# Optimization experiments

Measured on AMD Instinct MI355X. Metric: run time of the kernel, lower is better.

## Reference

```python
import jax, jax.numpy as jnp
import numpy as np


def setup_inputs() -> dict:
    key = jax.random.key(0)
    ks = jax.random.split(key, 5)
    B, T, S, D = 4, 32, 320, 768
    return {
        "x": jax.random.normal(ks[0], (B, T, S, D), dtype=jnp.float32),
        "qkv_w": jax.random.normal(ks[1], (D, 3 * D), dtype=jnp.float32) * 0.02,
        "qkv_b": jax.random.normal(ks[2], (3 * D,), dtype=jnp.float32) * 0.02,
        "out_w": jax.random.normal(ks[3], (D, D), dtype=jnp.float32) * 0.02,
        "out_b": jax.random.normal(ks[4], (D,), dtype=jnp.float32) * 0.02,
        "n_latents": 64,
        "n_heads": 12,
    }


def reference(x, qkv_w, qkv_b, out_w, out_b, n_latents, n_heads):
    B, T, S, D = x.shape
    H = n_heads
    hd = D // H
    scale = 1.0 / jnp.sqrt(jnp.asarray(hd, dtype=x.dtype))

    # qkv projection: [B,T,S,3D]
    qkv = jnp.einsum('btsd,de->btse', x, qkv_w) + qkv_b
    q, k, v = jnp.split(qkv, 3, axis=-1)
    # [B,T,S,H,hd]
    q = q.reshape(B, T, S, H, hd)
    k = k.reshape(B, T, S, H, hd)
    v = v.reshape(B, T, S, H, hd)

    # block-sparse mask: latent queries (rows < n_latents) cannot attend to
    # patch keys (cols >= n_latents); everything else allowed
    rows = jnp.arange(S) < n_latents          # latent query rows
    cols = jnp.arange(S) >= n_latents         # patch key cols
    allow = ~(rows[:, None] & cols[None, :])  # [S,S] bool

    # attention scores [B,T,H,Sq,Sk]
    scores = jnp.einsum('btqhd,btkhd->bthqk', q, k) * scale
    scores = jnp.where(allow, scores, -jnp.inf)
    attn = jax.nn.softmax(scores, axis=-1)

    y = jnp.einsum('bthqk,btkhd->btqhd', attn, v).reshape(B, T, S, D)
    return jnp.einsum('btsd,de->btse', y, out_w) + out_b
```

## Files before the change

kernel.cpp:

```cpp
#include <hip/hip_runtime.h>

typedef __attribute__((ext_vector_type(8))) short bf16x8;
typedef __attribute__((ext_vector_type(4))) float f32x4;
typedef __attribute__((ext_vector_type(16))) float f32x16;
typedef __attribute__((address_space(1))) void gvoid_t;
typedef __attribute__((address_space(3))) void lvoid_t;

#define DEVI __device__ __forceinline__
#define SB __builtin_amdgcn_sched_barrier(0)

DEVI unsigned short f2bf(float f) {
    unsigned int u = __builtin_bit_cast(unsigned int, f);
    u += 0x7fffu + ((u >> 16) & 1u);
    return (unsigned short)(u >> 16);
}

DEVI unsigned cvt_pk_bf16(float a, float b) {
    unsigned r;
    asm("v_cvt_pk_bf16_f32 %0, %1, %2" : "=v"(r) : "v"(a), "v"(b));
    return r;
}

DEVI f32x4 mfma16(bf16x8 a, bf16x8 b, f32x4 c) {
    return __builtin_amdgcn_mfma_f32_16x16x32_bf16(a, b, c, 0, 0, 0);
}

__global__ void k_convert(const float* __restrict__ in, unsigned short* __restrict__ out, int n8) {
    int i = blockIdx.x * 256 + threadIdx.x;
    if (i >= n8) return;
    const float4* p = (const float4*)in + (size_t)i * 2;
    float4 a = p[0], b = p[1];
    uint4 o;
    o.x = f2bf(a.x) | ((unsigned)f2bf(a.y) << 16);
    o.y = f2bf(a.z) | ((unsigned)f2bf(a.w) << 16);
    o.z = f2bf(b.x) | ((unsigned)f2bf(b.y) << 16);
    o.w = f2bf(b.z) | ((unsigned)f2bf(b.w) << 16);
    *((uint4*)out + i) = o;
}

__global__ void k_transpose(const float* __restrict__ w, unsigned short* __restrict__ wt, int K, int N) {
    __shared__ float tile[32][33];
    int n0 = blockIdx.x * 32, k0 = blockIdx.y * 32;
    int tx = threadIdx.x, ty = threadIdx.y;
#pragma unroll
    for (int r = 0; r < 32; r += 8)
        tile[ty + r][tx] = w[(size_t)(k0 + ty + r) * N + n0 + tx];
    __syncthreads();
#pragma unroll
    for (int r = 0; r < 32; r += 8)
        wt[(size_t)(n0 + ty + r) * K + k0 + tx] = f2bf(tile[tx][ty + r]);
}

__global__ __launch_bounds__(256) void k_kpack(const unsigned short* __restrict__ qkv,
                                               unsigned short* __restrict__ kp) {
    int bht = blockIdx.x;
    int t = bht % 10, bh = bht / 10;
    int h = bh % 12, bt = bh / 12;
    int c = threadIdx.x >> 6, l = threadIdx.x & 63;
    const unsigned short* src = qkv + (size_t)(bt * 320 + t * 32 + (l & 31)) * 2304
                                + 768 + h * 64 + c * 16 + (l >> 5) * 8;
    uint4 v = *(const uint4*)src;
    *(uint4*)(kp + ((size_t)bht * 4 + c) * 512 + l * 8) = v;
}

template <bool OUT_BF16>
__global__ __launch_bounds__(512, 2) void k_gemm256(const unsigned short* __restrict__ A,
                                                    const unsigned short* __restrict__ Bt,
                                                    const float* __restrict__ bias,
                                                    void* __restrict__ out,
                                                    int M, int N, int K) {
    __shared__ unsigned short smem[65536];

    const int tid = threadIdx.x;
    const int nwg = gridDim.x, bid = blockIdx.x;
    const int q8 = nwg >> 3, r8 = nwg & 7;
    const int xcd = bid & 7, lid = bid >> 3;
    const int swz = ((xcd < r8) ? xcd * (q8 + 1) : r8 * (q8 + 1) + (xcd - r8) * q8) + lid;
    const int ntn = N >> 8;
    const int bm = swz / ntn, bn = swz % ntn;

    const int lane = tid & 63, wid = tid >> 6;
    const int wr = wid >> 2, wc = wid & 3;
    const int lr = lane & 15, lg = lane >> 4;
    const int cswz = (lr & 7) << 3;
    const int col0 = (lg * 8) ^ cswz;

    const int NT = K >> 6;

    const int srowl = tid >> 3;
    const int scole = ((tid & 7) ^ (srowl & 7)) << 3;
    const unsigned short* aSrc = A  + (size_t)(bm * 256 + srowl) * K + scole;
    const unsigned short* bSrc = Bt + (size_t)(bn * 256 + srowl) * K + scole;

#define STG(matOff, srcBase, qq, koff, bufw)                                              \
    __builtin_amdgcn_global_load_lds((gvoid_t*)((srcBase) + (size_t)(qq) * 64 * K + (koff)), \
        (lvoid_t*)(smem + (matOff) + (bufw) * 16384 + (qq) * 4096 + tid * 8), 16, 0, 0)
#define LDA(mf, base, rowoff, kk) \
    *(const bf16x8*)((base) + ((rowoff) + (mf) * 16 + lr) * 64 + (col0 ^ ((kk) * 32)))

    f32x4 acc[8][4];
#pragma unroll
    for (int i = 0; i < 8; ++i)
#pragma unroll
        for (int j = 0; j < 4; ++j) acc[i][j] = (f32x4){0.f, 0.f, 0.f, 0.f};

    {
        const int k1 = (NT > 1) ? 64 : 0;
        STG(0, aSrc, 0, 0, 0); STG(0, aSrc, 1, 0, 0); STG(0, aSrc, 2, 0, 0); STG(0, aSrc, 3, 0, 0);
        STG(32768, bSrc, 0, 0, 0); STG(32768, bSrc, 1, 0, 0); STG(32768, bSrc, 2, 0, 0); STG(32768, bSrc, 3, 0, 0);
        STG(0, aSrc, 0, k1, 1); STG(0, aSrc, 2, k1, 1);
        asm volatile("s_waitcnt vmcnt(2)" ::: "memory");
        __builtin_amdgcn_s_barrier();
    }

#pragma unroll 1
    for (int t = 0; t < NT; ++t) {
        const int bufR = t & 1, bufW = bufR ^ 1;
        const int ko1 = (t + 1 < NT) ? (t + 1) * 64 : 0;
        const int ko2 = (t + 2 < NT) ? (t + 2) * 64 : 0;
        const unsigned short* abuf = smem + bufR * 16384;
        const unsigned short* bbuf = smem + 32768 + bufR * 16384;
        bf16x8 afv[4][2], b01[2][2], b23[2][2];

#pragma unroll
        for (int j = 0; j < 2; ++j)
#pragma unroll
            for (int kk = 0; kk < 2; ++kk)
                b01[j][kk] = LDA(j, bbuf, wc * 64, kk);
#pragma unroll
        for (int mf = 0; mf < 2; ++mf)
#pragma unroll
            for (int kk = 0; kk < 2; ++kk)
                afv[mf][kk] = LDA(mf, abuf, wr * 128, kk);
        SB;
#pragma unroll
        for (int mf = 2; mf < 4; ++mf)
#pragma unroll
            for (int kk = 0; kk < 2; ++kk)
                afv[mf][kk] = LDA(mf, abuf, wr * 128, kk);
        SB;
        STG(32768, bSrc, 0, ko1, bufW); STG(32768, bSrc, 1, ko1, bufW);
        STG(32768, bSrc, 2, ko1, bufW); STG(32768, bSrc, 3, ko1, bufW);
        STG(0, aSrc, 1, ko1, bufW); STG(0, aSrc, 3, ko1, bufW);
        asm volatile("s_waitcnt lgkmcnt(4)" ::: "memory"); SB;
        __builtin_amdgcn_s_setprio(1);
#pragma unroll
        for (int mf = 0; mf < 2; ++mf)
#pragma unroll
            for (int j = 0; j < 2; ++j)
#pragma unroll
                for (int kk = 0; kk < 2; ++kk)
                    acc[mf][j] = mfma16(afv[mf][kk], b01[j][kk], acc[mf][j]);
        __builtin_amdgcn_s_setprio(0);
        asm volatile("s_waitcnt lgkmcnt(0)" ::: "memory"); SB;
        __builtin_amdgcn_s_setprio(1);
#pragma unroll
        for (int mf = 2; mf < 4; ++mf)
#pragma unroll
            for (int j = 0; j < 2; ++j)
#pragma unroll
                for (int kk = 0; kk < 2; ++kk)
                    acc[mf][j] = mfma16(afv[mf][kk], b01[j][kk], acc[mf][j]);
        __builtin_amdgcn_s_setprio(0);

#pragma unroll
        for (int kk = 0; kk < 2; ++kk)
            b23[0][kk] = LDA(2, bbuf, wc * 64, kk);
        SB;
#pragma unroll
        for (int kk = 0; kk < 2; ++kk)
            b23[1][kk] = LDA(3, bbuf, wc * 64, kk);
        SB;
        asm volatile("s_waitcnt lgkmcnt(2)" ::: "memory"); SB;
        __builtin_amdgcn_s_setprio(1);
#pragma unroll
        for (int mf = 0; mf < 4; ++mf)
#pragma unroll
            for (int kk = 0; kk < 2; ++kk)
                acc[mf][2] = mfma16(afv[mf][kk], b23[0][kk], acc[mf][2]);
        __builtin_amdgcn_s_setprio(0);
        asm volatile("s_waitcnt lgkmcnt(0)" ::: "memory"); SB;
        __builtin_amdgcn_s_setprio(1);
#pragma unroll
        for (int mf = 0; mf < 4; ++mf)
#pragma unroll
            for (int kk = 0; kk < 2; ++kk)
                acc[mf][3] = mfma16(afv[mf][kk], b23[1][kk], acc[mf][3]);
        __builtin_amdgcn_s_setprio(0);

#pragma unroll
        for (int mf = 0; mf < 2; ++mf)
#pragma unroll
            for (int kk = 0; kk < 2; ++kk)
                afv[mf][kk] = LDA(mf, abuf, wr * 128 + 64, kk);
        SB;
#pragma unroll
        for (int mf = 2; mf < 4; ++mf)
#pragma unroll
            for (int kk = 0; kk < 2; ++kk)
                afv[mf][kk] = LDA(mf, abuf, wr * 128 + 64, kk);
        SB;
        asm volatile("s_waitcnt lgkmcnt(4)" ::: "memory"); SB;
        __builtin_amdgcn_s_setprio(1);
#pragma unroll
        for (int mf = 0; mf < 2; ++mf)
#pragma unroll
            for (int j = 0; j < 2; ++j)
#pragma unroll
                for (int kk = 0; kk < 2; ++kk)
                    acc[4 + mf][2 + j] = mfma16(afv[mf][kk], b23[j][kk], acc[4 + mf][2 + j]);
        __builtin_amdgcn_s_setprio(0);
        asm volatile("s_waitcnt lgkmcnt(0)" ::: "memory"); SB;
        __builtin_amdgcn_s_setprio(1);
#pragma unroll
        for (int mf = 2; mf < 4; ++mf)
#pragma unroll
            for (int j = 0; j < 2; ++j)
#pragma unroll
                for (int kk = 0; kk < 2; ++kk)
                    acc[4 + mf][2 + j] = mfma16(afv[mf][kk], b23[j][kk], acc[4 + mf][2 + j]);
        __builtin_amdgcn_s_setprio(0);

        __builtin_amdgcn_s_setprio(1);
#pragma unroll
        for (int mf = 0; mf < 4; ++mf)
#pragma unroll
            for (int j = 0; j < 2; ++j)
#pragma unroll
                for (int kk = 0; kk < 2; ++kk)
                    acc[4 + mf][j] = mfma16(afv[mf][kk], b01[j][kk], acc[4 + mf][j]);
        __builtin_amdgcn_s_setprio(0);
        asm volatile("s_waitcnt vmcnt(0)" ::: "memory");
        __builtin_amdgcn_s_barrier();
        STG(0, aSrc, 0, ko2, bufR); STG(0, aSrc, 2, ko2, bufR);
    }
#undef STG
#undef LDA

    asm volatile("s_waitcnt vmcnt(0)" ::: "memory");
    __syncthreads();
    float bv[4];
#pragma unroll
    for (int nf = 0; nf < 4; ++nf)
        bv[nf] = bias[bn * 256 + wc * 64 + nf * 16 + lr];

    if (OUT_BF16) {
        unsigned short* ebuf = smem + wid * 8192;
#pragma unroll
        for (int h = 0; h < 2; ++h) {
#pragma unroll
            for (int mf4 = 0; mf4 < 4; ++mf4) {
                int mf = h * 4 + mf4;
#pragma unroll
                for (int nf = 0; nf < 4; ++nf)
#pragma unroll
                    for (int i = 0; i < 4; ++i)
                        ebuf[(mf4 * 16 + lg * 4 + i) * 72 + nf * 16 + lr] = f2bf(acc[mf][nf][i] + bv[nf]);
            }
            asm volatile("s_waitcnt lgkmcnt(0)" ::: "memory"); SB;
#pragma unroll
            for (int ps = 0; ps < 8; ++ps) {
                int rl = ps * 8 + (lane >> 3), ck = lane & 7;
                uint4 vv = *(const uint4*)&ebuf[rl * 72 + ck * 8];
                int grow = bm * 256 + wr * 128 + h * 64 + rl;
                int gcol = bn * 256 + wc * 64 + ck * 8;
                *(uint4*)&((unsigned short*)out)[(size_t)grow * N + gcol] = vv;
            }
            asm volatile("s_waitcnt lgkmcnt(0)" ::: "memory"); SB;
        }
    } else {
        float* ebuf = (float*)smem + wid * 4096;
#pragma unroll
        for (int qq = 0; qq < 4; ++qq) {
#pragma unroll
            for (int m2 = 0; m2 < 2; ++m2) {
                int mf = qq * 2 + m2;
#pragma unroll
                for (int nf = 0; nf < 4; ++nf)
#pragma unroll
                    for (int i = 0; i < 4; ++i)
                        ebuf[(m2 * 16 + lg * 4 + i) * 68 + nf * 16 + lr] = acc[mf][nf][i] + bv[nf];
            }
            asm volatile("s_waitcnt lgkmcnt(0)" ::: "memory"); SB;
#pragma unroll
            for (int ps = 0; ps < 8; ++ps) {
                int rl = ps * 4 + (lane >> 4), ck = lane & 15;
                uint4 vv = *(const uint4*)&ebuf[rl * 68 + ck * 4];
                int grow = bm * 256 + wr * 128 + qq * 32 + rl;
                int gcol = bn * 256 + wc * 64 + ck * 4;
                *(uint4*)&((float*)out)[(size_t)grow * N + gcol] = vv;
            }
            asm volatile("s_waitcnt lgkmcnt(0)" ::: "memory"); SB;
        }
    }
}

__global__ __launch_bounds__(640, 5) void k_attn6(const unsigned short* __restrict__ qkv,
                                                  const unsigned short* __restrict__ kp,
                                                  unsigned short* __restrict__ y) {
    int bt = blockIdx.x / 12, h = blockIdx.x % 12;
    const unsigned short* Qg = qkv + (size_t)bt * 320 * 2304 + h * 64;
    const unsigned short* Vg = Qg + 1536;
    const unsigned short* Kpb = kp + (size_t)blockIdx.x * 20480;

    __shared__ unsigned short Vt[10 * 64 * 40];

    int tid = threadIdx.x, w = tid >> 6, l = tid & 63;
    int q = l & 31, hh = l >> 5;
    int q0 = w * 32;
    int ntile = (w < 2) ? 2 : 10;

#pragma unroll
    for (int it = 0; it < 2; ++it) {
        int blk = tid + it * 640;
        int tt = blk >> 7, rr = blk & 127;
        int k0 = (rr & 7) * 4;
        int d0 = (rr >> 3) * 4;
        const unsigned short* src = Vg + (size_t)(tt * 32 + k0) * 2304 + d0;
        union { uint2 u; unsigned short s[4]; } r0, r1, r2, r3;
        r0.u = *(const uint2*)(src);
        r1.u = *(const uint2*)(src + 2304);
        r2.u = *(const uint2*)(src + 4608);
        r3.u = *(const uint2*)(src + 6912);
#pragma unroll
        for (int dd = 0; dd < 4; ++dd) {
            int d = d0 + dd;
            int sw = ((d >> 3) & 3) << 3;
            uint2 o;
            o.x = (unsigned)r0.s[dd] | ((unsigned)r1.s[dd] << 16);
            o.y = (unsigned)r2.s[dd] | ((unsigned)r3.s[dd] << 16);
            *(uint2*)&Vt[(size_t)(tt * 64 + d) * 40 + (k0 ^ sw)] = o;
        }
    }

    bf16x8 qf[4];
#pragma unroll
    for (int c = 0; c < 4; ++c)
        qf[c] = *(const bf16x8*)(Qg + (size_t)(q0 + q) * 2304 + c * 16 + hh * 8);

    f32x16 o0 = (f32x16)0.f, o1 = (f32x16)0.f;
    float m = -3e38f, lsum = 0.f;
    const float SC = 0.125f * 1.44269504089f;

    __syncthreads();

    for (int t = 0; t < ntile; ++t) {
        bf16x8 kf[4];
#pragma unroll
        for (int c = 0; c < 4; ++c)
            kf[c] = *(const bf16x8*)(Kpb + t * 2048 + c * 512 + l * 8);

        f32x16 sacc = (f32x16)0.f;
#pragma unroll
        for (int c = 0; c < 4; ++c)
            sacc = __builtin_amdgcn_mfma_f32_32x32x16_bf16(kf[c], qf[c], sacc, 0, 0, 0);

        float p[16];
#pragma unroll
        for (int r = 0; r < 16; ++r) p[r] = sacc[r] * SC;
        float tm = fmaxf(
            fmaxf(fmaxf(fmaxf(p[0], p[1]), fmaxf(p[2], p[3])),
                  fmaxf(fmaxf(p[4], p[5]), fmaxf(p[6], p[7]))),
            fmaxf(fmaxf(fmaxf(p[8], p[9]), fmaxf(p[10], p[11])),
                  fmaxf(fmaxf(p[12], p[13]), fmaxf(p[14], p[15]))));
        tm = fmaxf(tm, __shfl_xor(tm, 32));
        if (!__all(tm <= m + 8.f)) {
            float mn = fmaxf(m, tm);
            float al = __builtin_amdgcn_exp2f(m - mn);
            lsum *= al;
#pragma unroll
            for (int r = 0; r < 16; ++r) { o0[r] *= al; o1[r] *= al; }
            m = mn;
        }
#pragma unroll
        for (int r = 0; r < 16; ++r) p[r] = __builtin_amdgcn_exp2f(p[r] - m);
        float rs =
            ((p[0] + p[1]) + (p[2] + p[3])) + ((p[4] + p[5]) + (p[6] + p[7])) +
            (((p[8] + p[9]) + (p[10] + p[11])) + ((p[12] + p[13]) + (p[14] + p[15])));
        lsum += rs;

        unsigned a0 = cvt_pk_bf16(p[0], p[1]);
        unsigned a1 = cvt_pk_bf16(p[2], p[3]);
        unsigned b0 = cvt_pk_bf16(p[4], p[5]);
        unsigned b1 = cvt_pk_bf16(p[6], p[7]);
        asm("v_permlane32_swap_b32 %0, %1" : "+v"(a0), "+v"(b0));
        asm("v_permlane32_swap_b32 %0, %1" : "+v"(a1), "+v"(b1));
        unsigned c0 = cvt_pk_bf16(p[8], p[9]);
        unsigned c1 = cvt_pk_bf16(p[10], p[11]);
        unsigned d0 = cvt_pk_bf16(p[12], p[13]);
        unsigned d1 = cvt_pk_bf16(p[14], p[15]);
        asm("v_permlane32_swap_b32 %0, %1" : "+v"(c0), "+v"(d0));
        asm("v_permlane32_swap_b32 %0, %1" : "+v"(c1), "+v"(d1));
        union { unsigned u[4]; bf16x8 v; } pf0, pf1;
        pf0.u[0] = a0; pf0.u[1] = a1; pf0.u[2] = b0; pf0.u[3] = b1;
        pf1.u[0] = c0; pf1.u[1] = c1; pf1.u[2] = d0; pf1.u[3] = d1;

        const unsigned short* vt = Vt + t * 2560;
        {
            int d = q;
            int sw = (d >> 3) & 3;
            bf16x8 va0 = *(const bf16x8*)&vt[d * 40 + ((0 + hh) ^ sw) * 8];
            bf16x8 va1 = *(const bf16x8*)&vt[d * 40 + ((2 + hh) ^ sw) * 8];
            o0 = __builtin_amdgcn_mfma_f32_32x32x16_bf16(va0, pf0.v, o0, 0, 0, 0);
            o0 = __builtin_amdgcn_mfma_f32_32x32x16_bf16(va1, pf1.v, o0, 0, 0, 0);
        }
        {
            int d = 32 + q;
            int sw = (d >> 3) & 3;
            bf16x8 va0 = *(const bf16x8*)&vt[d * 40 + ((0 + hh) ^ sw) * 8];
            bf16x8 va1 = *(const bf16x8*)&vt[d * 40 + ((2 + hh) ^ sw) * 8];
            o1 = __builtin_amdgcn_mfma_f32_32x32x16_bf16(va0, pf0.v, o1, 0, 0, 0);
            o1 = __builtin_amdgcn_mfma_f32_32x32x16_bf16(va1, pf1.v, o1, 0, 0, 0);
        }
    }

    lsum += __shfl_xor(lsum, 32);
    float inv = 1.f / lsum;
    unsigned short* yp = y + (size_t)(bt * 320 + q0 + q) * 768 + h * 64;
#pragma unroll
    for (int r = 0; r < 16; r += 2) {
        int dr = (r & 3) + 8 * (r >> 2) + 4 * hh;
        *(unsigned*)(yp + dr) =
            (unsigned)f2bf(o0[r] * inv) | ((unsigned)f2bf(o0[r + 1] * inv) << 16);
        *(unsigned*)(yp + 32 + dr) =
            (unsigned)f2bf(o1[r] * inv) | ((unsigned)f2bf(o1[r + 1] * inv) << 16);
    }
}

extern "C" void kernel_launch(void* const* d_in, const int* in_sizes, int n_in,
                              void* d_out, int out_size, void* d_ws, size_t ws_size,
                              hipStream_t stream) {
    const float* x     = (const float*)d_in[0];
    const float* qkv_w = (const float*)d_in[1];
    const float* qkv_b = (const float*)d_in[2];
    const float* out_w = (const float*)d_in[3];
    const float* out_b = (const float*)d_in[4];

    const int M = 40960;
    unsigned short* xb  = (unsigned short*)d_ws;
    unsigned short* w1t = xb + (size_t)M * 768;
    unsigned short* w2t = w1t + (size_t)2304 * 768;
    unsigned short* qkv = w2t + (size_t)768 * 768;
    unsigned short* yb  = qkv + (size_t)M * 2304;
    unsigned short* kp  = xb;

    k_convert<<<(M * 768 / 8 + 255) / 256, 256, 0, stream>>>(x, xb, M * 768 / 8);
    k_transpose<<<dim3(2304 / 32, 768 / 32), dim3(32, 8), 0, stream>>>(qkv_w, w1t, 768, 2304);
    k_transpose<<<dim3(768 / 32, 768 / 32), dim3(32, 8), 0, stream>>>(out_w, w2t, 768, 768);

    k_gemm256<true><<<(M / 256) * (2304 / 256), 512, 0, stream>>>(xb, w1t, qkv_b, (void*)qkv, M, 2304, 768);
    k_kpack<<<1536 * 10, 256, 0, stream>>>(qkv, kp);
    k_attn6<<<128 * 12, 640, 0, stream>>>(qkv, kp, yb);
    k_gemm256<false><<<(M / 256) * (768 / 256), 512, 0, stream>>>(yb, w2t, out_b, d_out, M, 768, 768);
}
```

Before: 384.0 us.

## Restructure GEMM main loop with B-fragment prefetch and drop K-pack kernel

The GEMM inner loop is reorganised into a two-tile unrolled lambda. It loads all A-low fragments up front and prefetches the next tile's B0 fragments from the other LDS buffer after the barrier, so LDS reads overlap with MFMA work. Separately, the k_kpack launch is removed and the attention kernel reads K directly from the strided qkv buffer. This saves one kernel launch and a full pass over K, at the cost of less coalesced K loads inside attention. The unroll-by-two assumes NT is even (768/64=12), and holding more fragments live raises register pressure.

```diff
diff --git a/kernel.cpp b/kernel.cpp
--- a/kernel.cpp
+++ b/kernel.cpp
@@ -51,18 +51,6 @@
         wt[(size_t)(n0 + ty + r) * K + k0 + tx] = f2bf(tile[tx][ty + r]);
 }
 
-__global__ __launch_bounds__(256) void k_kpack(const unsigned short* __restrict__ qkv,
-                                               unsigned short* __restrict__ kp) {
-    int bht = blockIdx.x;
-    int t = bht % 10, bh = bht / 10;
-    int h = bh % 12, bt = bh / 12;
-    int c = threadIdx.x >> 6, l = threadIdx.x & 63;
-    const unsigned short* src = qkv + (size_t)(bt * 320 + t * 32 + (l & 31)) * 2304
-                                + 768 + h * 64 + c * 16 + (l >> 5) * 8;
-    uint4 v = *(const uint4*)src;
-    *(uint4*)(kp + ((size_t)bht * 4 + c) * 512 + l * 8) = v;
-}
-
 template <bool OUT_BF16>
 __global__ __launch_bounds__(512, 2) void k_gemm256(const unsigned short* __restrict__ A,
                                                     const unsigned short* __restrict__ Bt,
@@ -104,6 +92,8 @@
 #pragma unroll
         for (int j = 0; j < 4; ++j) acc[i][j] = (f32x4){0.f, 0.f, 0.f, 0.f};
 
+    bf16x8 b0A[2][2], b0B[2][2];
+
     {
         const int k1 = (NT > 1) ? 64 : 0;
         STG(0, aSrc, 0, 0, 0); STG(0, aSrc, 1, 0, 0); STG(0, aSrc, 2, 0, 0); STG(0, aSrc, 3, 0, 0);
@@ -111,33 +101,32 @@
         STG(0, aSrc, 0, k1, 1); STG(0, aSrc, 2, k1, 1);
         asm volatile("s_waitcnt vmcnt(2)" ::: "memory");
         __builtin_amdgcn_s_barrier();
-    }
-
-#pragma unroll 1
-    for (int t = 0; t < NT; ++t) {
+#pragma unroll
+        for (int j = 0; j < 2; ++j)
+#pragma unroll
+            for (int kk = 0; kk < 2; ++kk)
+                b0A[j][kk] = LDA(j, smem + 32768, wc * 64, kk);
+    }
+
+    auto TILE = [&](int t, bf16x8 (&b0c)[2][2], bf16x8 (&b0n)[2][2]) {
         const int bufR = t & 1, bufW = bufR ^ 1;
         const int ko1 = (t + 1 < NT) ? (t + 1) * 64 : 0;
         const int ko2 = (t + 2 < NT) ? (t + 2) * 64 : 0;
         const unsigned short* abuf = smem + bufR * 16384;
         const unsigned short* bbuf = smem + 32768 + bufR * 16384;
-        bf16x8 afv[4][2], b01[2][2], b23[2][2];
-
+        const unsigned short* bbufN = smem + 32768 + bufW * 16384;
+        bf16x8 a_lo[4][2], a_hi[4][2], b1[2][2];
+
+#pragma unroll
+        for (int mf = 0; mf < 4; ++mf)
+#pragma unroll
+            for (int kk = 0; kk < 2; ++kk)
+                a_lo[mf][kk] = LDA(mf, abuf, wr * 128, kk);
 #pragma unroll
         for (int j = 0; j < 2; ++j)
 #pragma unroll
             for (int kk = 0; kk < 2; ++kk)
-                b01[j][kk] = LDA(j, bbuf, wc * 64, kk);
-#pragma unroll
-        for (int mf = 0; mf < 2; ++mf)
-#pragma unroll
-            for (int kk = 0; kk < 2; ++kk)
-                afv[mf][kk] = LDA(mf, abuf, wr * 128, kk);
-        SB;
-#pragma unroll
-        for (int mf = 2; mf < 4; ++mf)
-#pragma unroll
-            for (int kk = 0; kk < 2; ++kk)
-                afv[mf][kk] = LDA(mf, abuf, wr * 128, kk);
+                b1[j][kk] = LDA(2 + j, bbuf, wc * 64, kk);
         SB;
         STG(32768, bSrc, 0, ko1, bufW); STG(32768, bSrc, 1, ko1, bufW);
         STG(32768, bSrc, 2, ko1, bufW); STG(32768, bSrc, 3, ko1, bufW);
@@ -145,99 +134,71 @@
         asm volatile("s_waitcnt lgkmcnt(4)" ::: "memory"); SB;
         __builtin_amdgcn_s_setprio(1);
 #pragma unroll
-        for (int mf = 0; mf < 2; ++mf)
+        for (int mf = 0; mf < 4; ++mf)
 #pragma unroll
             for (int j = 0; j < 2; ++j)
 #pragma unroll
                 for (int kk = 0; kk < 2; ++kk)
-                    acc[mf][j] = mfma16(afv[mf][kk], b01[j][kk], acc[mf][j]);
+                    acc[mf][j] = mfma16(a_lo[mf][kk], b0c[j][kk], acc[mf][j]);
         __builtin_amdgcn_s_setprio(0);
         asm volatile("s_waitcnt lgkmcnt(0)" ::: "memory"); SB;
+
+#pragma unroll
+        for (int mf = 0; mf < 4; ++mf)
+#pragma unroll
+            for (int kk = 0; kk < 2; ++kk)
+                a_hi[mf][kk] = LDA(mf, abuf, wr * 128 + 64, kk);
+        SB;
         __builtin_amdgcn_s_setprio(1);
 #pragma unroll
-        for (int mf = 2; mf < 4; ++mf)
+        for (int mf = 0; mf < 4; ++mf)
 #pragma unroll
             for (int j = 0; j < 2; ++j)
 #pragma unroll
                 for (int kk = 0; kk < 2; ++kk)
-                    acc[mf][j] = mfma16(afv[mf][kk], b01[j][kk], acc[mf][j]);
-        __builtin_amdgcn_s_setprio(0);
-
-#pragma unroll
-        for (int kk = 0; kk < 2; ++kk)
-            b23[0][kk] = LDA(2, bbuf, wc * 64, kk);
-        SB;
-#pragma unroll
-        for (int kk = 0; kk < 2; ++kk)
-            b23[1][kk] = LDA(3, bbuf, wc * 64, kk);
-        SB;
-        asm volatile("s_waitcnt lgkmcnt(2)" ::: "memory"); SB;
-        __builtin_amdgcn_s_setprio(1);
-#pragma unroll
-        for (int mf = 0; mf < 4; ++mf)
-#pragma unroll
-            for (int kk = 0; kk < 2; ++kk)
-                acc[mf][2] = mfma16(afv[mf][kk], b23[0][kk], acc[mf][2]);
+                    acc[mf][2 + j] = mfma16(a_lo[mf][kk], b1[j][kk], acc[mf][2 + j]);
         __builtin_amdgcn_s_setprio(0);
         asm volatile("s_waitcnt lgkmcnt(0)" ::: "memory"); SB;
+
         __builtin_amdgcn_s_setprio(1);
 #pragma unroll
         for (int mf = 0; mf < 4; ++mf)
 #pragma unroll
-            for (int kk = 0; kk < 2; ++kk)
-                acc[mf][3] = mfma16(afv[mf][kk], b23[1][kk], acc[mf][3]);
-        __builtin_amdgcn_s_setprio(0);
-
-#pragma unroll
-        for (int mf = 0; mf < 2; ++mf)
-#pragma unroll
-            for (int kk = 0; kk < 2; ++kk)
-                afv[mf][kk] = LDA(mf, abuf, wr * 128 + 64, kk);
-        SB;
-#pragma unroll
-        for (int mf = 2; mf < 4; ++mf)
-#pragma unroll
-            for (int kk = 0; kk < 2; ++kk)
-                afv[mf][kk] = LDA(mf, abuf, wr * 128 + 64, kk);
-        SB;
-        asm volatile("s_waitcnt lgkmcnt(4)" ::: "memory"); SB;
-        __builtin_amdgcn_s_setprio(1);
-#pragma unroll
-        for (int mf = 0; mf < 2; ++mf)
-#pragma unroll
             for (int j = 0; j < 2; ++j)
 #pragma unroll
                 for (int kk = 0; kk < 2; ++kk)
-                    acc[4 + mf][2 + j] = mfma16(afv[mf][kk], b23[j][kk], acc[4 + mf][2 + j]);
-        __builtin_amdgcn_s_setprio(0);
-        asm volatile("s_waitcnt lgkmcnt(0)" ::: "memory"); SB;
-        __builtin_amdgcn_s_setprio(1);
-#pragma unroll
-        for (int mf = 2; mf < 4; ++mf)
-#pragma unroll
-            for (int j = 0; j < 2; ++j)
-#pragma unroll
-                for (int kk = 0; kk < 2; ++kk)
-                    acc[4 + mf][2 + j] = mfma16(afv[mf][kk], b23[j][kk], acc[4 + mf][2 + j]);
-        __builtin_amdgcn_s_setprio(0);
-
-        __builtin_amdgcn_s_setprio(1);
-#pragma unroll
-        for (int mf = 0; mf < 4; ++mf)
-#pragma unroll
-            for (int j = 0; j < 2; ++j)
-#pragma unroll
-                for (int kk = 0; kk < 2; ++kk)
-                    acc[4 + mf][j] = mfma16(afv[mf][kk], b01[j][kk], acc[4 + mf][j]);
+                    acc[4 + mf][2 + j] = mfma16(a_hi[mf][kk], b1[j][kk], acc[4 + mf][2 + j]);
         __builtin_amdgcn_s_setprio(0);
         asm volatile("s_waitcnt vmcnt(0)" ::: "memory");
         __builtin_amdgcn_s_barrier();
+
+#pragma unroll
+        for (int j = 0; j < 2; ++j)
+#pragma unroll
+            for (int kk = 0; kk < 2; ++kk)
+                b0n[j][kk] = LDA(j, bbufN, wc * 64, kk);
+        SB;
         STG(0, aSrc, 0, ko2, bufR); STG(0, aSrc, 2, ko2, bufR);
+        __builtin_amdgcn_s_setprio(1);
+#pragma unroll
+        for (int mf = 0; mf < 4; ++mf)
+#pragma unroll
+            for (int j = 0; j < 2; ++j)
+#pragma unroll
+                for (int kk = 0; kk < 2; ++kk)
+                    acc[4 + mf][j] = mfma16(a_hi[mf][kk], b0c[j][kk], acc[4 + mf][j]);
+        __builtin_amdgcn_s_setprio(0);
+    };
+
+#pragma unroll 1
+    for (int t = 0; t < NT; t += 2) {
+        TILE(t, b0A, b0B);
+        TILE(t + 1, b0B, b0A);
     }
 #undef STG
 #undef LDA
 
-    asm volatile("s_waitcnt vmcnt(0)" ::: "memory");
+    asm volatile("s_waitcnt vmcnt(0) lgkmcnt(0)" ::: "memory");
     __syncthreads();
     float bv[4];
 #pragma unroll
@@ -296,12 +257,11 @@
 }
 
 __global__ __launch_bounds__(640, 5) void k_attn6(const unsigned short* __restrict__ qkv,
-                                                  const unsigned short* __restrict__ kp,
                                                   unsigned short* __restrict__ y) {
     int bt = blockIdx.x / 12, h = blockIdx.x % 12;
     const unsigned short* Qg = qkv + (size_t)bt * 320 * 2304 + h * 64;
+    const unsigned short* Kg = Qg + 768;
     const unsigned short* Vg = Qg + 1536;
-    const unsigned short* Kpb = kp + (size_t)blockIdx.x * 20480;
 
     __shared__ unsigned short Vt[10 * 64 * 40];
 
@@ -348,7 +308,7 @@
         bf16x8 kf[4];
 #pragma unroll
         for (int c = 0; c < 4; ++c)
-            kf[c] = *(const bf16x8*)(Kpb + t * 2048 + c * 512 + l * 8);
+            kf[c] = *(const bf16x8*)(Kg + (size_t)(t * 32 + q) * 2304 + c * 16 + hh * 8);
 
         f32x16 sacc = (f32x16)0.f;
 #pragma unroll
@@ -442,14 +402,12 @@
     unsigned short* w2t = w1t + (size_t)2304 * 768;
     unsigned short* qkv = w2t + (size_t)768 * 768;
     unsigned short* yb  = qkv + (size_t)M * 2304;
-    unsigned short* kp  = xb;
 
     k_convert<<<(M * 768 / 8 + 255) / 256, 256, 0, stream>>>(x, xb, M * 768 / 8);
     k_transpose<<<dim3(2304 / 32, 768 / 32), dim3(32, 8), 0, stream>>>(qkv_w, w1t, 768, 2304);
     k_transpose<<<dim3(768 / 32, 768 / 32), dim3(32, 8), 0, stream>>>(out_w, w2t, 768, 768);
 
     k_gemm256<true><<<(M / 256) * (2304 / 256), 512, 0, stream>>>(xb, w1t, qkv_b, (void*)qkv, M, 2304, 768);
-    k_kpack<<<1536 * 10, 256, 0, stream>>>(qkv, kp);
-    k_attn6<<<128 * 12, 640, 0, stream>>>(qkv, kp, yb);
+    k_attn6<<<128 * 12, 640, 0, stream>>>(qkv, yb);
     k_gemm256<false><<<(M / 256) * (768 / 256), 512, 0, stream>>>(yb, w2t, out_b, d_out, M, 768, 768);
 }
```

New measurement: 399.6 us. 1.04x slower.
